# Kernel optimization log

Hardware: AMD Instinct MI355X
Metric: run time of the kernel (lower is better)

The kernel has to match this reference:

```python
import jax, jax.numpy as jnp
import numpy as np


def setup_inputs() -> dict:
    key = jax.random.key(0)
    k1, k2, k3 = jax.random.split(key, 3)
    B, S, N = 32, 128, 256
    input_real = jax.random.normal(k1, (B, S, N), dtype=jnp.float32)
    input_imag = jax.random.normal(k2, (B, S, N), dtype=jnp.float32)
    weight = jax.random.uniform(k3, (B, S), dtype=jnp.float32)
    return {"input_real": input_real, "input_imag": input_imag, "weight": weight}


def reference(input_real, input_imag, weight):
    # Weighted mixture of rank-1 density matrices over the sequence dim S.
    # output_real[b,n,m] = sum_s w[b,s] * (r[b,s,n]*r[b,s,m] + i[b,s,n]*i[b,s,m])
    # output_imag[b,n,m] = sum_s w[b,s] * (i[b,s,n]*r[b,s,m] - r[b,s,n]*i[b,s,m])
    # Fused: pre-scale one factor by the weight, then a single contraction over S
    # (never materializes the [B,S,N,N] intermediates of the torch code).
    wr = input_real * weight[:, :, None]  # [B,S,N]
    wi = input_imag * weight[:, :, None]  # [B,S,N]
    output_r = jnp.einsum('bsn,bsm->bnm', wr, input_real) + jnp.einsum('bsn,bsm->bnm', wi, input_imag)
    output_i = jnp.einsum('bsn,bsm->bnm', wi, input_real) - jnp.einsum('bsn,bsm->bnm', wr, input_imag)
    return (output_r, output_i)
```

## Files before the change

### kernel.cpp

```cpp
#include <hip/hip_runtime.h>
#include <hip/hip_fp16.h>


constexpr int B = 32, S = 128, N = 256;

typedef _Float16 f16x8  __attribute__((ext_vector_type(8)));
typedef float    f32x16 __attribute__((ext_vector_type(16)));

union F16x8 { f16x8 v; __half2 h2[4]; };

#define MFMA32(a, bv, c) __builtin_amdgcn_mfma_f32_32x32x16_f16((a), (bv), (c), 0, 0, 0)

#define LBAR() {                                                             \
        __builtin_amdgcn_sched_barrier(0);                                   \
        asm volatile("s_waitcnt lgkmcnt(0)" ::: "memory");                   \
        __builtin_amdgcn_s_barrier();                                        \
        __builtin_amdgcn_sched_barrier(0); }

__global__ __launch_bounds__(512, 2) void ComplexMixture_71313636983193_kernel(
    const float* __restrict__ R, const float* __restrict__ I,
    const float* __restrict__ W, float* __restrict__ Or, float* __restrict__ Oi)
{
    __shared__ alignas(16) _Float16 T[6][64][128];

    const int pb   = blockIdx.x;
    const int lbid = (pb & 7) * 32 + (pb >> 3);
    const int b   = lbid >> 3;
    const int rem = lbid & 7;
    const int ti  = rem >> 1;
    const int uu  = rem & 1;
    const int tj1 = uu * 2, tj2 = uu * 2 + 1;

    const int t  = threadIdx.x;
    const int wv = t >> 6, lane = t & 63;

    const int nquad = t & 15;
    const int octet = (t >> 4) & 15;
    const int arr   = t >> 8;
    const int s0    = octet * 8;

    const size_t bb = (size_t)b * S * N;
    const float* base  = (arr ? I : R) + bb + nquad * 4;
    const float* srcA  = base + ti  * 64;
    const float* srcB1 = base + tj1 * 64;
    const float* Wb = W + b * S;

    float4 fA[8], fB1[8];
    #pragma unroll
    for (int s = 0; s < 8; ++s)
        fA[s] = *(const float4*)&srcA[(size_t)(s0 + s) * N];
    #pragma unroll
    for (int s = 0; s < 8; ++s)
        fB1[s] = *(const float4*)&srcB1[(size_t)(s0 + s) * N];

    float w8[8];
    {
        const float4 a0 = *(const float4*)&Wb[s0];
        const float4 a1 = *(const float4*)&Wb[s0 + 4];
        w8[0]=a0.x; w8[1]=a0.y; w8[2]=a0.z; w8[3]=a0.w;
        w8[4]=a1.x; w8[5]=a1.y; w8[6]=a1.z; w8[7]=a1.w;
    }

    #pragma unroll
    for (int j = 0; j < 4; ++j) {
        const int n    = nquad * 4 + j;
        const int slot = octet ^ ((n >> 1) & 7);
        F16x8 fa, fb;
        #pragma unroll
        for (int k = 0; k < 4; ++k) {
            fa.h2[k] = __floats2half2_rn(((const float*)&fA[2*k])[j]   * w8[2*k],
                                         ((const float*)&fA[2*k+1])[j] * w8[2*k+1]);
            fb.h2[k] = __floats2half2_rn(((const float*)&fB1[2*k])[j],
                                         ((const float*)&fB1[2*k+1])[j]);
        }
        *(f16x8*)&T[arr][n][slot * 8]     = fa.v;
        *(f16x8*)&T[2 + arr][n][slot * 8] = fb.v;
    }

    float4 fB2R[8], fB2I[8];
    if (wv >= 4) {
        const float* sR = R + bb + tj2 * 64 + nquad * 4;
        const float* sI = I + bb + tj2 * 64 + nquad * 4;
        #pragma unroll
        for (int s = 0; s < 8; ++s)
            fB2R[s] = *(const float4*)&sR[(size_t)(s0 + s) * N];
        #pragma unroll
        for (int s = 0; s < 8; ++s)
            fB2I[s] = *(const float4*)&sI[(size_t)(s0 + s) * N];
    }

    LBAR();

    const int sn = (wv >> 1) & 1;
    const int sm = wv & 1;
    const int l31 = lane & 31, hi = lane >> 5;
    const int rowA = sn * 32 + l31;    const int sgA = (rowA >> 1) & 7;
    const int rowB = sm * 32 + l31;    const int sgB = (rowB >> 1) & 7;

    f32x16 dR = {0,0,0,0,0,0,0,0,0,0,0,0,0,0,0,0};
    f32x16 dA = {0,0,0,0,0,0,0,0,0,0,0,0,0,0,0,0};
    f32x16 dB = {0,0,0,0,0,0,0,0,0,0,0,0,0,0,0,0};

#define FRAG_STEP(TB, ks) {                                                  \
        const int ca = ((2 * (ks) + hi) ^ sgA) * 8;                          \
        const int cb = ((2 * (ks) + hi) ^ sgB) * 8;                          \
        const f16x8 ar = *(const f16x8*)&T[0][rowA][ca];                     \
        const f16x8 ai = *(const f16x8*)&T[1][rowA][ca];                     \
        const f16x8 br = *(const f16x8*)&T[TB][rowB][cb];                    \
        const f16x8 bi = *(const f16x8*)&T[(TB) + 1][rowB][cb];              \
        dR = MFMA32(ar, br, dR); dR = MFMA32(ai, bi, dR);                    \
        dA = MFMA32(ai, br, dA); dB = MFMA32(ar, bi, dB); }

#define STORE_TILE(TJ) {                                                     \
        const int mm = (TJ) * 64 + sm * 32 + l31;                            \
        _Pragma("unroll")                                                    \
        for (int r = 0; r < 16; ++r) {                                       \
            const int nn = ti * 64 + sn * 32 + (r & 3) + 8 * (r >> 2) + 4 * hi; \
            const size_t o = ((size_t)b * N + nn) * N + mm;                  \
            Or[o] = dR[r];                                                   \
            Oi[o] = dA[r] - dB[r];                                           \
        } }

    if (wv < 4) {
        __builtin_amdgcn_s_setprio(1);
        FRAG_STEP(2, 0); FRAG_STEP(2, 1); FRAG_STEP(2, 2); FRAG_STEP(2, 3);
        FRAG_STEP(2, 4); FRAG_STEP(2, 5); FRAG_STEP(2, 6); FRAG_STEP(2, 7);
        __builtin_amdgcn_s_setprio(0);
    } else {
        #pragma unroll
        for (int j = 0; j < 4; ++j) {
            const int n    = nquad * 4 + j;
            const int slot = octet ^ ((n >> 1) & 7);
            F16x8 fr, fi;
            #pragma unroll
            for (int k = 0; k < 4; ++k) {
                fr.h2[k] = __floats2half2_rn(((const float*)&fB2R[2*k])[j],
                                             ((const float*)&fB2R[2*k+1])[j]);
                fi.h2[k] = __floats2half2_rn(((const float*)&fB2I[2*k])[j],
                                             ((const float*)&fB2I[2*k+1])[j]);
            }
            *(f16x8*)&T[4][n][slot * 8] = fr.v;
            *(f16x8*)&T[5][n][slot * 8] = fi.v;
        }
    }

    LBAR();

    if (wv < 4) {
        STORE_TILE(tj1);
    } else {
        __builtin_amdgcn_s_setprio(1);
        FRAG_STEP(4, 0); FRAG_STEP(4, 1); FRAG_STEP(4, 2); FRAG_STEP(4, 3);
        FRAG_STEP(4, 4); FRAG_STEP(4, 5); FRAG_STEP(4, 6); FRAG_STEP(4, 7);
        __builtin_amdgcn_s_setprio(0);
        STORE_TILE(tj2);
    }
}

extern "C" void kernel_launch(void* const* d_in, const int* in_sizes, int n_in,
                              void* d_out, int out_size, void* d_ws, size_t ws_size,
                              hipStream_t stream) {
    const float* R = (const float*)d_in[0];
    const float* I = (const float*)d_in[1];
    const float* W = (const float*)d_in[2];
    float* Or = (float*)d_out;
    float* Oi = (float*)d_out + (size_t)B * N * N;

    ComplexMixture_71313636983193_kernel<<<dim3(256), dim3(512), 0, stream>>>(
        R, I, W, Or, Oi);
}
```

Measured before the change: 13.28 us.

## Retile to 128x64 output per block with S split into two pipelined halves

Each block now computes a 128(n) x 64(m) output tile, where it previously computed one 64-row tile against two 64-column tiles in sequence. The S=128 reduction is split into two halves: the second half's global loads are issued before the first-half MFMAs and converted into LDS afterward, overlapping loading with compute. All 8 waves work on the same phases, removing the earlier split where half the waves sat idle, and the real-part output stores are issued before the final imaginary MFMAs so writeback overlaps them. The cost is more LDS for the larger A tile and idle lanes during B loads, since only half the threads load B.

```diff
diff --git a/kernel.cpp b/kernel.cpp
--- a/kernel.cpp
+++ b/kernel.cpp
@@ -21,78 +21,93 @@
     const float* __restrict__ R, const float* __restrict__ I,
     const float* __restrict__ W, float* __restrict__ Or, float* __restrict__ Oi)
 {
-    __shared__ alignas(16) _Float16 T[6][64][128];
+    __shared__ alignas(16) _Float16 AW[2][128][128];
+    __shared__ alignas(16) _Float16 Bt[2][64][128];
 
     const int pb   = blockIdx.x;
     const int lbid = (pb & 7) * 32 + (pb >> 3);
     const int b   = lbid >> 3;
     const int rem = lbid & 7;
-    const int ti  = rem >> 1;
-    const int uu  = rem & 1;
-    const int tj1 = uu * 2, tj2 = uu * 2 + 1;
+    const int nh  = rem >> 2;
+    const int mj  = rem & 3;
 
     const int t  = threadIdx.x;
     const int wv = t >> 6, lane = t & 63;
 
-    const int nquad = t & 15;
-    const int octet = (t >> 4) & 15;
     const int arr   = t >> 8;
-    const int s0    = octet * 8;
+    const int u     = t & 255;
+    const int nquad = u >> 3;
+    const int octet = u & 7;
+    const bool doB  = (u < 128);
+    const int mquad = u >> 3;
 
     const size_t bb = (size_t)b * S * N;
-    const float* base  = (arr ? I : R) + bb + nquad * 4;
-    const float* srcA  = base + ti  * 64;
-    const float* srcB1 = base + tj1 * 64;
-    const float* Wb = W + b * S;
-
-    float4 fA[8], fB1[8];
+    const float* arrp = arr ? I : R;
+    const float* srcA = arrp + bb + nh * 128 + nquad * 4;
+    const float* srcB = arrp + bb + mj * 64 + mquad * 4;
+    const float* Wb   = W + b * S;
+
+    float4 fA[8], fB[8];
     #pragma unroll
     for (int s = 0; s < 8; ++s)
-        fA[s] = *(const float4*)&srcA[(size_t)(s0 + s) * N];
-    #pragma unroll
-    for (int s = 0; s < 8; ++s)
-        fB1[s] = *(const float4*)&srcB1[(size_t)(s0 + s) * N];
-
-    float w8[8];
+        fA[s] = *(const float4*)&srcA[(size_t)(octet * 8 + s) * N];
+    if (doB) {
+        #pragma unroll
+        for (int s = 0; s < 8; ++s)
+            fB[s] = *(const float4*)&srcB[(size_t)(octet * 8 + s) * N];
+    }
+
+    float w0[8], w1[8];
     {
-        const float4 a0 = *(const float4*)&Wb[s0];
-        const float4 a1 = *(const float4*)&Wb[s0 + 4];
-        w8[0]=a0.x; w8[1]=a0.y; w8[2]=a0.z; w8[3]=a0.w;
-        w8[4]=a1.x; w8[5]=a1.y; w8[6]=a1.z; w8[7]=a1.w;
+        const float4 a0 = *(const float4*)&Wb[octet * 8];
+        const float4 a1 = *(const float4*)&Wb[octet * 8 + 4];
+        const float4 a2 = *(const float4*)&Wb[64 + octet * 8];
+        const float4 a3 = *(const float4*)&Wb[64 + octet * 8 + 4];
+        w0[0]=a0.x; w0[1]=a0.y; w0[2]=a0.z; w0[3]=a0.w;
+        w0[4]=a1.x; w0[5]=a1.y; w0[6]=a1.z; w0[7]=a1.w;
+        w1[0]=a2.x; w1[1]=a2.y; w1[2]=a2.z; w1[3]=a2.w;
+        w1[4]=a3.x; w1[5]=a3.y; w1[6]=a3.z; w1[7]=a3.w;
     }
 
     #pragma unroll
     for (int j = 0; j < 4; ++j) {
         const int n    = nquad * 4 + j;
         const int slot = octet ^ ((n >> 1) & 7);
-        F16x8 fa, fb;
-        #pragma unroll
-        for (int k = 0; k < 4; ++k) {
-            fa.h2[k] = __floats2half2_rn(((const float*)&fA[2*k])[j]   * w8[2*k],
-                                         ((const float*)&fA[2*k+1])[j] * w8[2*k+1]);
-            fb.h2[k] = __floats2half2_rn(((const float*)&fB1[2*k])[j],
-                                         ((const float*)&fB1[2*k+1])[j]);
+        F16x8 fa;
+        #pragma unroll
+        for (int k = 0; k < 4; ++k)
+            fa.h2[k] = __floats2half2_rn(((const float*)&fA[2*k])[j]   * w0[2*k],
+                                         ((const float*)&fA[2*k+1])[j] * w0[2*k+1]);
+        *(f16x8*)&AW[arr][n][slot * 8] = fa.v;
+    }
+    if (doB) {
+        #pragma unroll
+        for (int j = 0; j < 4; ++j) {
+            const int m    = mquad * 4 + j;
+            const int slot = octet ^ ((m >> 1) & 7);
+            F16x8 fb;
+            #pragma unroll
+            for (int k = 0; k < 4; ++k)
+                fb.h2[k] = __floats2half2_rn(((const float*)&fB[2*k])[j],
+                                             ((const float*)&fB[2*k+1])[j]);
+            *(f16x8*)&Bt[arr][m][slot * 8] = fb.v;
         }
-        *(f16x8*)&T[arr][n][slot * 8]     = fa.v;
-        *(f16x8*)&T[2 + arr][n][slot * 8] = fb.v;
-    }
-
-    float4 fB2R[8], fB2I[8];
-    if (wv >= 4) {
-        const float* sR = R + bb + tj2 * 64 + nquad * 4;
-        const float* sI = I + bb + tj2 * 64 + nquad * 4;
+    }
+
+    float4 gA[8], gB[8];
+    #pragma unroll
+    for (int s = 0; s < 8; ++s)
+        gA[s] = *(const float4*)&srcA[(size_t)(64 + octet * 8 + s) * N];
+    if (doB) {
         #pragma unroll
         for (int s = 0; s < 8; ++s)
-            fB2R[s] = *(const float4*)&sR[(size_t)(s0 + s) * N];
-        #pragma unroll
-        for (int s = 0; s < 8; ++s)
-            fB2I[s] = *(const float4*)&sI[(size_t)(s0 + s) * N];
+            gB[s] = *(const float4*)&srcB[(size_t)(64 + octet * 8 + s) * N];
     }
 
     LBAR();
 
-    const int sn = (wv >> 1) & 1;
-    const int sm = wv & 1;
+    const int sn = wv & 3;
+    const int sm = wv >> 2;
     const int l31 = lane & 31, hi = lane >> 5;
     const int rowA = sn * 32 + l31;    const int sgA = (rowA >> 1) & 7;
     const int rowB = sm * 32 + l31;    const int sgB = (rowB >> 1) & 7;
@@ -101,59 +116,73 @@
     f32x16 dA = {0,0,0,0,0,0,0,0,0,0,0,0,0,0,0,0};
     f32x16 dB = {0,0,0,0,0,0,0,0,0,0,0,0,0,0,0,0};
 
-#define FRAG_STEP(TB, ks) {                                                  \
+#define FRAG_STEP(ks) {                                                      \
         const int ca = ((2 * (ks) + hi) ^ sgA) * 8;                          \
         const int cb = ((2 * (ks) + hi) ^ sgB) * 8;                          \
-        const f16x8 ar = *(const f16x8*)&T[0][rowA][ca];                     \
-        const f16x8 ai = *(const f16x8*)&T[1][rowA][ca];                     \
-        const f16x8 br = *(const f16x8*)&T[TB][rowB][cb];                    \
-        const f16x8 bi = *(const f16x8*)&T[(TB) + 1][rowB][cb];              \
+        const f16x8 ar = *(const f16x8*)&AW[0][rowA][ca];                    \
+        const f16x8 ai = *(const f16x8*)&AW[1][rowA][ca];                    \
+        const f16x8 br = *(const f16x8*)&Bt[0][rowB][cb];                    \
+        const f16x8 bi = *(const f16x8*)&Bt[1][rowB][cb];                    \
         dR = MFMA32(ar, br, dR); dR = MFMA32(ai, bi, dR);                    \
         dA = MFMA32(ai, br, dA); dB = MFMA32(ar, bi, dB); }
 
-#define STORE_TILE(TJ) {                                                     \
-        const int mm = (TJ) * 64 + sm * 32 + l31;                            \
-        _Pragma("unroll")                                                    \
-        for (int r = 0; r < 16; ++r) {                                       \
-            const int nn = ti * 64 + sn * 32 + (r & 3) + 8 * (r >> 2) + 4 * hi; \
-            const size_t o = ((size_t)b * N + nn) * N + mm;                  \
-            Or[o] = dR[r];                                                   \
-            Oi[o] = dA[r] - dB[r];                                           \
-        } }
-
-    if (wv < 4) {
-        __builtin_amdgcn_s_setprio(1);
-        FRAG_STEP(2, 0); FRAG_STEP(2, 1); FRAG_STEP(2, 2); FRAG_STEP(2, 3);
-        FRAG_STEP(2, 4); FRAG_STEP(2, 5); FRAG_STEP(2, 6); FRAG_STEP(2, 7);
-        __builtin_amdgcn_s_setprio(0);
-    } else {
+    __builtin_amdgcn_s_setprio(1);
+    FRAG_STEP(0); FRAG_STEP(1); FRAG_STEP(2); FRAG_STEP(3);
+    __builtin_amdgcn_s_setprio(0);
+
+    #pragma unroll
+    for (int j = 0; j < 4; ++j) {
+        const int n    = nquad * 4 + j;
+        const int slot = (8 + octet) ^ ((n >> 1) & 7);
+        F16x8 fa;
+        #pragma unroll
+        for (int k = 0; k < 4; ++k)
+            fa.h2[k] = __floats2half2_rn(((const float*)&gA[2*k])[j]   * w1[2*k],
+                                         ((const float*)&gA[2*k+1])[j] * w1[2*k+1]);
+        *(f16x8*)&AW[arr][n][slot * 8] = fa.v;
+    }
+    if (doB) {
         #pragma unroll
         for (int j = 0; j < 4; ++j) {
-            const int n    = nquad * 4 + j;
-            const int slot = octet ^ ((n >> 1) & 7);
-            F16x8 fr, fi;
+            const int m    = mquad * 4 + j;
+            const int slot = (8 + octet) ^ ((m >> 1) & 7);
+            F16x8 fb;
             #pragma unroll
-            for (int k = 0; k < 4; ++k) {
-                fr.h2[k] = __floats2half2_rn(((const float*)&fB2R[2*k])[j],
-                                             ((const float*)&fB2R[2*k+1])[j]);
-                fi.h2[k] = __floats2half2_rn(((const float*)&fB2I[2*k])[j],
-                                             ((const float*)&fB2I[2*k+1])[j]);
-            }
-            *(f16x8*)&T[4][n][slot * 8] = fr.v;
-            *(f16x8*)&T[5][n][slot * 8] = fi.v;
+            for (int k = 0; k < 4; ++k)
+                fb.h2[k] = __floats2half2_rn(((const float*)&gB[2*k])[j],
+                                             ((const float*)&gB[2*k+1])[j]);
+            *(f16x8*)&Bt[arr][m][slot * 8] = fb.v;
         }
     }
 
     LBAR();
 
-    if (wv < 4) {
-        STORE_TILE(tj1);
-    } else {
-        __builtin_amdgcn_s_setprio(1);
-        FRAG_STEP(4, 0); FRAG_STEP(4, 1); FRAG_STEP(4, 2); FRAG_STEP(4, 3);
-        FRAG_STEP(4, 4); FRAG_STEP(4, 5); FRAG_STEP(4, 6); FRAG_STEP(4, 7);
-        __builtin_amdgcn_s_setprio(0);
-        STORE_TILE(tj2);
+    __builtin_amdgcn_s_setprio(1);
+    FRAG_STEP(4); FRAG_STEP(5); FRAG_STEP(6);
+    const int ca7 = ((2 * 7 + hi) ^ sgA) * 8;
+    const int cb7 = ((2 * 7 + hi) ^ sgB) * 8;
+    const f16x8 ar7 = *(const f16x8*)&AW[0][rowA][ca7];
+    const f16x8 ai7 = *(const f16x8*)&AW[1][rowA][ca7];
+    const f16x8 br7 = *(const f16x8*)&Bt[0][rowB][cb7];
+    const f16x8 bi7 = *(const f16x8*)&Bt[1][rowB][cb7];
+    dR = MFMA32(ar7, br7, dR); dR = MFMA32(ai7, bi7, dR);
+    __builtin_amdgcn_s_setprio(0);
+
+    const int mm = mj * 64 + sm * 32 + l31;
+    #pragma unroll
+    for (int r = 0; r < 16; ++r) {
+        const int nn = nh * 128 + sn * 32 + (r & 3) + 8 * (r >> 2) + 4 * hi;
+        Or[((size_t)b * N + nn) * N + mm] = dR[r];
+    }
+
+    __builtin_amdgcn_s_setprio(1);
+    dA = MFMA32(ai7, br7, dA); dB = MFMA32(ar7, bi7, dB);
+    __builtin_amdgcn_s_setprio(0);
+
+    #pragma unroll
+    for (int r = 0; r < 16; ++r) {
+        const int nn = nh * 128 + sn * 32 + (r & 3) + 8 * (r >> 2) + 4 * hi;
+        Oi[((size_t)b * N + nn) * N + mm] = dA[r] - dB[r];
     }
 }
 
```

Measured after the change: 16.71 us. 1.26x slower.
